# Performance work log

Hardware: AMD Instinct MI355X
Metric: run time of the kernel (lower is better)

Reference implementation:

```python
import jax, jax.numpy as jnp
from jax import lax
import numpy as np

B, N, C, T = 64, 25, 128, 256
EPS = 1e-5


def setup_inputs() -> dict:
    key = jax.random.key(0)
    ks = jax.random.split(key, 4)
    x = jax.random.normal(ks[0], (B, N, C, T), dtype=jnp.float32)
    adj = jax.random.uniform(ks[1], (N, N), dtype=jnp.float32)
    # row-normalize adjacency like a typical GCN propagation matrix
    adj = adj / jnp.sum(adj, axis=1, keepdims=True)
    # xavier-uniform-ish linear weight [out, in]
    lim = float(np.sqrt(6.0 / (C + C)))
    W_gcn = jax.random.uniform(ks[2], (C, C), minval=-lim, maxval=lim, dtype=jnp.float32)
    b_gcn = jnp.zeros((C,), jnp.float32)
    W_conv = jax.random.normal(ks[3], (C, C, 3), dtype=jnp.float32) * (1.0 / np.sqrt(3 * C))
    b_conv = jnp.zeros((C,), jnp.float32)
    return dict(
        x=x, adj=adj, W_gcn=W_gcn, b_gcn=b_gcn, W_conv=W_conv, b_conv=b_conv,
        tc_gamma=jnp.ones((C,), jnp.float32), tc_beta=jnp.zeros((C,), jnp.float32),
        tc_mean=jnp.zeros((C,), jnp.float32), tc_var=jnp.ones((C,), jnp.float32),
        bn_gamma=jnp.ones((C,), jnp.float32), bn_beta=jnp.zeros((C,), jnp.float32),
        bn_mean=jnp.zeros((C,), jnp.float32), bn_var=jnp.ones((C,), jnp.float32),
    )


def _bn(x, gamma, beta, mean, var, axis):
    # eval-mode batchnorm over channel `axis`
    shape = [1] * x.ndim
    shape[axis] = -1
    g = gamma.reshape(shape)
    b = beta.reshape(shape)
    m = mean.reshape(shape)
    v = var.reshape(shape)
    return g * (x - m) * lax.rsqrt(v + EPS) + b


def reference(x, adj, W_gcn, b_gcn, W_conv, b_conv,
              tc_gamma, tc_beta, tc_mean, tc_var,
              bn_gamma, bn_beta, bn_mean, bn_var):
    # x: [B, N, C, T]; in_channels == out_channels so residual is identity
    b_, n_, c_, t_ = x.shape
    residual = x
    # spatial GCN for all timesteps at once: linear over feature dim, then adj matmul over nodes
    h = jnp.einsum('bnct,oc->bnot', x, W_gcn) + b_gcn[None, None, :, None]
    h = jnp.einsum('mn,bnot->bmot', adj, h)  # [B, N, C, T]
    # temporal conv1d over T for every (batch, node) pair at once
    hc = h.reshape(b_ * n_, c_, t_)
    y = lax.conv_general_dilated(hc, W_conv, window_strides=(1,), padding=[(1, 1)],
                                 dimension_numbers=('NCH', 'OIH', 'NCH'))
    y = y + b_conv[None, :, None]
    y = _bn(y, tc_gamma, tc_beta, tc_mean, tc_var, axis=1)
    y = jax.nn.relu(y)
    y = y.reshape(b_, n_, c_, t_)
    # residual add, block batchnorm over channels, relu
    y = y + residual
    y = _bn(y, bn_gamma, bn_beta, bn_mean, bn_var, axis=2)
    y = jax.nn.relu(y)
    return y
```

## Files before the change

### kernel.cpp

```cpp
#include <hip/hip_runtime.h>
#include <hip/hip_bf16.h>
#include <stdint.h>

#define Bn 64
#define Nn 25
#define Cn 128
#define Tn 256
#define EPSC 1e-5f

typedef short bf16x8 __attribute__((ext_vector_type(8)));
typedef float f32x4 __attribute__((ext_vector_type(4)));
typedef int   i32x4 __attribute__((ext_vector_type(4)));

static constexpr size_t X2T_BYTES  = (size_t)Bn * Nn * Tn * Cn * 2;
static constexpr size_t WEFF_OFF   = X2T_BYTES;
static constexpr size_t WEFF_BYTES = (size_t)3 * 128 * 128 * 2;
static constexpr size_t EPI_OFF    = WEFF_OFF + WEFF_BYTES;
static constexpr size_t ROWSUM_OFF = EPI_OFF + (size_t)7 * 128 * 4;
static constexpr size_t ZPAGE_OFF  = ROWSUM_OFF + 256;
static constexpr size_t WS_NEEDED  = ZPAGE_OFF + 256;

__device__ __forceinline__ uint16_t f2bf(float f) {
    uint32_t u = __builtin_bit_cast(uint32_t, f);
    u = (u + 0x7FFFu + ((u >> 16) & 1u)) >> 16;
    return (uint16_t)u;
}

__device__ __forceinline__ void dma16(const void* gsrc, void* ldst) {
    __builtin_amdgcn_global_load_lds(
        (const __attribute__((address_space(1))) unsigned int*)gsrc,
        (__attribute__((address_space(3))) unsigned int*)ldst, 16, 0, 0);
}

__global__ __launch_bounds__(128) void prep_kernel(
    const float* __restrict__ adj, const float* __restrict__ Wg,
    const float* __restrict__ bg,  const float* __restrict__ Wc,
    const float* __restrict__ bc,
    const float* __restrict__ tg,  const float* __restrict__ tb_,
    const float* __restrict__ tm,  const float* __restrict__ tv,
    const float* __restrict__ bng, const float* __restrict__ bnb,
    const float* __restrict__ bnm, const float* __restrict__ bnv,
    uint16_t* __restrict__ weff, float* __restrict__ epi, float* __restrict__ rowsum,
    uint32_t* __restrict__ zpage)
{
    int blk = blockIdx.x;
    int tid = threadIdx.x;
    if (blk < 384) {
        int k = blk >> 7, o = blk & 127;
        float acc = 0.f;
        for (int i = 0; i < 128; ++i) {
            float wc = Wc[(o * 128 + i) * 3 + k];
            acc = fmaf(wc, Wg[i * 128 + tid], acc);
        }
        weff[((size_t)(k * 128 + o)) * 128 + tid] = f2bf(acc);
    } else {
        int o = tid;
        float b0 = 0.f, b1 = 0.f, b2 = 0.f;
        for (int i = 0; i < 128; ++i) {
            float g = bg[i];
            b0 = fmaf(Wc[(o * 128 + i) * 3 + 0], g, b0);
            b1 = fmaf(Wc[(o * 128 + i) * 3 + 1], g, b1);
            b2 = fmaf(Wc[(o * 128 + i) * 3 + 2], g, b2);
        }
        float a1  = tg[o] * rsqrtf(tv[o] + EPSC);
        float c1p = tb_[o] - a1 * tm[o] + a1 * bc[o];
        float a2  = bng[o] * rsqrtf(bnv[o] + EPSC);
        float c2  = bnb[o] - a2 * bnm[o];
        epi[0 * 128 + o] = a1;
        epi[1 * 128 + o] = c1p;
        epi[2 * 128 + o] = a2;
        epi[3 * 128 + o] = c2;
        epi[4 * 128 + o] = a1 * b0;
        epi[5 * 128 + o] = a1 * b1;
        epi[6 * 128 + o] = a1 * b2;
        if (tid < Nn) {
            float s = 0.f;
            for (int n = 0; n < Nn; ++n) s += adj[tid * Nn + n];
            rowsum[tid] = s;
        }
        if (tid < 64) zpage[tid] = 0u;
    }
}

__global__ __launch_bounds__(256) void adjmix_kernel(
    const float* __restrict__ x, const float* __restrict__ adj,
    uint16_t* __restrict__ x2t)
{
    __shared__ float adjs[Nn * Nn];
    __shared__ float tr[2][2][32][33];

    int bid = blockIdx.x;
    int b  = bid >> 5;
    int rem = bid & 31;
    int cb = rem >> 3, tb = rem & 7;
    int c0 = cb * 32, t0 = tb * 32;
    int tid = threadIdx.x;

    for (int i = tid; i < Nn * Nn; i += 256) adjs[i] = adj[i];
    __syncthreads();

    int cl = tid >> 3;
    int t4 = (tid & 7) * 4;

    float acc[Nn][4];
#pragma unroll
    for (int m = 0; m < Nn; ++m)
#pragma unroll
        for (int j = 0; j < 4; ++j) acc[m][j] = 0.f;

    for (int n = 0; n < Nn; ++n) {
        const float4 v = *reinterpret_cast<const float4*>(
            x + (((size_t)(b * Nn + n) * Cn + c0 + cl) * Tn + t0 + t4));
#pragma unroll
        for (int m = 0; m < Nn; ++m) {
            float a = adjs[m * Nn + n];
            acc[m][0] = fmaf(a, v.x, acc[m][0]);
            acc[m][1] = fmaf(a, v.y, acc[m][1]);
            acc[m][2] = fmaf(a, v.z, acc[m][2]);
            acc[m][3] = fmaf(a, v.w, acc[m][3]);
        }
    }

    int h    = tid & 127;
    int half = tid >> 7;
    int trow = h >> 2;
    int cq   = h & 3;

#pragma unroll
    for (int p = 0; p < 13; ++p) {
        int m0  = 2 * p;
        int buf = p & 1;
#pragma unroll
        for (int j = 0; j < 4; ++j) tr[buf][0][cl][t4 + j] = acc[m0][j];
        if (m0 + 1 < Nn) {
#pragma unroll
            for (int j = 0; j < 4; ++j) tr[buf][1][cl][t4 + j] = acc[m0 + 1][j];
        }
        __syncthreads();
        int mm = m0 + half;
        if (mm < Nn) {
            i32x4 u;
#pragma unroll
            for (int k2 = 0; k2 < 4; ++k2) {
                uint32_t lo16 = f2bf(tr[buf][half][cq * 8 + 2 * k2 + 0][trow]);
                uint32_t hi16 = f2bf(tr[buf][half][cq * 8 + 2 * k2 + 1][trow]);
                u[k2] = (int)(lo16 | (hi16 << 16));
            }
            size_t elem = ((size_t)(b * Nn + mm) * Tn + (t0 + trow)) * Cn + c0 + cq * 8;
            *reinterpret_cast<i32x4*>(x2t + elem) = u;
        }
    }
}

__global__ __launch_bounds__(256, 2) void conv_kernel(
    const uint16_t* __restrict__ x2t, const uint16_t* __restrict__ weff,
    const float* __restrict__ x, const float* __restrict__ epi,
    const float* __restrict__ rowsum, const char* __restrict__ zpage,
    float* __restrict__ out)
{
    constexpr int ROWB = 256;
    constexpr int BUFB = 34 * ROWB;
    __shared__ uint16_t lds[2 * 34 * 128];
    char* ldsb = (char*)lds;

    int bid = blockIdx.x;
    int bm  = bid >> 1;
    int th  = bid & 1;
    int m   = bm % Nn;
    int T0  = th * 128;

    int tid = threadIdx.x;
    int w  = tid >> 6;
    int l  = tid & 63;
    int lo = l & 15;
    int hi = l >> 4;
    int o0 = w * 32;

    const char*  xp2 = (const char*)x2t + (size_t)bm * Tn * Cn * 2;
    const short* wp  = (const short*)weff;

    bf16x8 bw[3][4][2];
#pragma unroll
    for (int kk = 0; kk < 3; ++kk)
#pragma unroll
        for (int cc = 0; cc < 4; ++cc)
#pragma unroll
            for (int f = 0; f < 2; ++f) {
                int o = o0 + f * 16 + lo;
                bw[kk][cc][f] = *reinterpret_cast<const bf16x8*>(
                    wp + ((size_t)(kk * 128 + o)) * 128 + cc * 32 + hi * 8);
            }

    float a1[2], c1[2], a2[2], c2v[2], g0[2], g1[2], g2[2];
#pragma unroll
    for (int f = 0; f < 2; ++f) {
        int o = o0 + f * 16 + lo;
        a1[f]  = epi[0 * 128 + o];
        c1[f]  = epi[1 * 128 + o];
        a2[f]  = epi[2 * 128 + o];
        c2v[f] = epi[3 * 128 + o];
        g0[f]  = epi[4 * 128 + o];
        g1[f]  = epi[5 * 128 + o];
        g2[f]  = epi[6 * 128 + o];
    }
    float rs = rowsum[m];
    const size_t obase = (size_t)bm * Cn;

    auto stage = [&](int it, int bufByte) {
        int t0 = T0 + it * 32;
#pragma unroll
        for (int oi = 0; oi < 2; ++oi) {
            int op = w + oi * 4;
            int rowbase = op * 4;
            int r  = rowbase + (l >> 4);
            int cg = l & 15;
            int gt = t0 - 1 + r;
            int sc = cg ^ (r & 7);
            const char* src = (gt >= 0 && gt < Tn)
                ? xp2 + ((size_t)gt * Cn + sc * 8) * 2
                : zpage + sc * 16;
            dma16(src, ldsb + bufByte + rowbase * ROWB);
        }
        if (w == 0 && l < 32) {
            int rowbase = 32;
            int r  = rowbase + (l >> 4);
            int cg = l & 15;
            int gt = t0 - 1 + r;
            int sc = cg ^ (r & 7);
            const char* src = (gt >= 0 && gt < Tn)
                ? xp2 + ((size_t)gt * Cn + sc * 8) * 2
                : zpage + sc * 16;
            dma16(src, ldsb + bufByte + rowbase * ROWB);
        }
    };

    int cur = 0;
    stage(0, 0);
    asm volatile("s_waitcnt vmcnt(0)" ::: "memory");
    __syncthreads();

    for (int it = 0; it < 4; ++it) {
        int nxt = cur ^ 1;
        if (it < 3) stage(it + 1, nxt * BUFB);

        int tq = T0 + it * 32;

        f32x4 r4[2][2];
        size_t idx4[2][2];
#pragma unroll
        for (int j = 0; j < 2; ++j)
#pragma unroll
            for (int f = 0; f < 2; ++f) {
                int o   = o0 + f * 16 + lo;
                int tb4 = tq + j * 16 + hi * 4;
                idx4[j][f] = (obase + o) * Tn + tb4;
                r4[j][f] = *reinterpret_cast<const f32x4*>(x + idx4[j][f]);
            }

        f32x4 acc[2][2];
#pragma unroll
        for (int j = 0; j < 2; ++j)
#pragma unroll
            for (int f = 0; f < 2; ++f) acc[j][f] = (f32x4){0.f, 0.f, 0.f, 0.f};

#pragma unroll
        for (int kk = 0; kk < 3; ++kk)
#pragma unroll
            for (int cc = 0; cc < 4; ++cc) {
                bf16x8 af[2];
#pragma unroll
                for (int j = 0; j < 2; ++j) {
                    int lrow  = j * 16 + lo + kk;
                    int lbyte = cur * BUFB + lrow * ROWB +
                                ((cc * 64 + hi * 16) ^ ((lrow & 7) << 4));
                    af[j] = *reinterpret_cast<const bf16x8*>(ldsb + lbyte);
                }
#pragma unroll
                for (int j = 0; j < 2; ++j)
#pragma unroll
                    for (int f = 0; f < 2; ++f)
                        acc[j][f] = __builtin_amdgcn_mfma_f32_16x16x32_bf16(
                            af[j], bw[kk][cc][f], acc[j][f], 0, 0, 0);
            }

        asm volatile("s_waitcnt vmcnt(0)" ::: "memory");
        __syncthreads();

#pragma unroll
        for (int j = 0; j < 2; ++j)
#pragma unroll
            for (int f = 0; f < 2; ++f) {
                int tb4 = tq + j * 16 + hi * 4;
                f32x4 ov;
#pragma unroll
                for (int qq = 0; qq < 4; ++qq) {
                    int t = tb4 + qq;
                    float gbv = g1[f];
                    if (t > 0)      gbv += g0[f];
                    if (t < Tn - 1) gbv += g2[f];
                    float z = fmaxf(fmaf(a1[f], acc[j][f][qq], fmaf(rs, gbv, c1[f])), 0.f);
                    ov[qq] = fmaxf(fmaf(a2[f], z + r4[j][f][qq], c2v[f]), 0.f);
                }
                *reinterpret_cast<f32x4*>(out + idx4[j][f]) = ov;
            }

        cur = nxt;
    }
}

extern "C" void kernel_launch(void* const* d_in, const int* in_sizes, int n_in,
                              void* d_out, int out_size, void* d_ws, size_t ws_size,
                              hipStream_t stream) {
    const float* x    = (const float*)d_in[0];
    const float* adj  = (const float*)d_in[1];
    const float* Wg   = (const float*)d_in[2];
    const float* bg   = (const float*)d_in[3];
    const float* Wc   = (const float*)d_in[4];
    const float* bc   = (const float*)d_in[5];
    const float* tg   = (const float*)d_in[6];
    const float* tb_  = (const float*)d_in[7];
    const float* tm   = (const float*)d_in[8];
    const float* tv   = (const float*)d_in[9];
    const float* bng  = (const float*)d_in[10];
    const float* bnb  = (const float*)d_in[11];
    const float* bnm  = (const float*)d_in[12];
    const float* bnv  = (const float*)d_in[13];

    if (ws_size < WS_NEEDED) return;

    char* ws = (char*)d_ws;
    uint16_t* x2t    = (uint16_t*)ws;
    uint16_t* weff   = (uint16_t*)(ws + WEFF_OFF);
    float*    epi    = (float*)(ws + EPI_OFF);
    float*    rowsum = (float*)(ws + ROWSUM_OFF);
    char*     zpage  = ws + ZPAGE_OFF;
    float*    out    = (float*)d_out;

    prep_kernel<<<385, 128, 0, stream>>>(adj, Wg, bg, Wc, bc, tg, tb_, tm, tv,
                                         bng, bnb, bnm, bnv, weff, epi, rowsum,
                                         (uint32_t*)zpage);
    adjmix_kernel<<<2048, 256, 0, stream>>>(x, adj, x2t);
    conv_kernel<<<Bn * Nn * 2, 256, 0, stream>>>(x2t, weff, x, epi, rowsum, zpage, out);
}
```

Before: 221.1 us.

## Triple-buffer conv LDS staging and process full time axis per block

Each conv block now covers all 256 timesteps of one (batch, node) pair instead of half, so the grid is halved and the per-block weight and epilogue setup is amortised over eight tiles. LDS staging goes from double to triple buffering with a prefetch distance of two tiles. The per-iteration full vmcnt(0) wait plus syncthreads becomes one raw s_barrier, relying on the in-order vector-memory counter that the compiler's wait on the residual loads already forces. The cost is fewer blocks in flight across the GPU, more LDS per block, and a subtle dependency on implicit wait ordering for correctness.

Measured after the change: 214.0 us. 3.2% less time.

```diff
diff --git a/kernel.cpp b/kernel.cpp
--- a/kernel.cpp
+++ b/kernel.cpp
@@ -160,14 +160,11 @@
 {
     constexpr int ROWB = 256;
     constexpr int BUFB = 34 * ROWB;
-    __shared__ uint16_t lds[2 * 34 * 128];
+    __shared__ uint16_t lds[3 * 34 * 128];
     char* ldsb = (char*)lds;
 
     int bid = blockIdx.x;
-    int bm  = bid >> 1;
-    int th  = bid & 1;
-    int m   = bm % Nn;
-    int T0  = th * 128;
+    int m   = bid % Nn;
 
     int tid = threadIdx.x;
     int w  = tid >> 6;
@@ -176,7 +173,7 @@
     int hi = l >> 4;
     int o0 = w * 32;
 
-    const char*  xp2 = (const char*)x2t + (size_t)bm * Tn * Cn * 2;
+    const char*  xp2 = (const char*)x2t + (size_t)bid * Tn * Cn * 2;
     const short* wp  = (const short*)weff;
 
     bf16x8 bw[3][4][2];
@@ -204,46 +201,46 @@
         g2[f]  = epi[6 * 128 + o];
     }
     float rs = rowsum[m];
-    const size_t obase = (size_t)bm * Cn;
-
-    auto stage = [&](int it, int bufByte) {
-        int t0 = T0 + it * 32;
+    const size_t obase = (size_t)bid * Cn;
+
+    auto stage = [&](int q, int slot) {
+        int tbase = q * 32 - 1;
+        char* dstbase = ldsb + slot * BUFB;
 #pragma unroll
         for (int oi = 0; oi < 2; ++oi) {
-            int op = w + oi * 4;
-            int rowbase = op * 4;
+            int rowbase = (w + oi * 4) * 4;
             int r  = rowbase + (l >> 4);
             int cg = l & 15;
-            int gt = t0 - 1 + r;
+            int gt = tbase + r;
             int sc = cg ^ (r & 7);
             const char* src = (gt >= 0 && gt < Tn)
                 ? xp2 + ((size_t)gt * Cn + sc * 8) * 2
                 : zpage + sc * 16;
-            dma16(src, ldsb + bufByte + rowbase * ROWB);
+            dma16(src, dstbase + rowbase * ROWB);
         }
         if (w == 0 && l < 32) {
             int rowbase = 32;
             int r  = rowbase + (l >> 4);
             int cg = l & 15;
-            int gt = t0 - 1 + r;
+            int gt = tbase + r;
             int sc = cg ^ (r & 7);
             const char* src = (gt >= 0 && gt < Tn)
                 ? xp2 + ((size_t)gt * Cn + sc * 8) * 2
                 : zpage + sc * 16;
-            dma16(src, ldsb + bufByte + rowbase * ROWB);
+            dma16(src, dstbase + rowbase * ROWB);
         }
     };
 
-    int cur = 0;
+    asm volatile("" ::: "memory");
     stage(0, 0);
-    asm volatile("s_waitcnt vmcnt(0)" ::: "memory");
-    __syncthreads();
-
-    for (int it = 0; it < 4; ++it) {
-        int nxt = cur ^ 1;
-        if (it < 3) stage(it + 1, nxt * BUFB);
-
-        int tq = T0 + it * 32;
+    stage(1, 1);
+    asm volatile("s_waitcnt vmcnt(2)" ::: "memory");
+    __builtin_amdgcn_s_barrier();
+    asm volatile("" ::: "memory");
+
+    int slot = 0;
+    for (int it = 0; it < 8; ++it) {
+        int tq = it * 32;
 
         f32x4 r4[2][2];
         size_t idx4[2][2];
@@ -256,6 +253,14 @@
                 idx4[j][f] = (obase + o) * Tn + tb4;
                 r4[j][f] = *reinterpret_cast<const f32x4*>(x + idx4[j][f]);
             }
+        __builtin_amdgcn_sched_barrier(0);
+
+        {
+            int q  = it + 2; if (q > 7) q = 7;
+            int s2 = slot >= 1 ? slot - 1 : 2;
+            stage(q, s2);
+        }
+        __builtin_amdgcn_sched_barrier(0);
 
         f32x4 acc[2][2];
 #pragma unroll
@@ -271,7 +276,7 @@
 #pragma unroll
                 for (int j = 0; j < 2; ++j) {
                     int lrow  = j * 16 + lo + kk;
-                    int lbyte = cur * BUFB + lrow * ROWB +
+                    int lbyte = slot * BUFB + lrow * ROWB +
                                 ((cc * 64 + hi * 16) ^ ((lrow & 7) << 4));
                     af[j] = *reinterpret_cast<const bf16x8*>(ldsb + lbyte);
                 }
@@ -282,9 +287,6 @@
                         acc[j][f] = __builtin_amdgcn_mfma_f32_16x16x32_bf16(
                             af[j], bw[kk][cc][f], acc[j][f], 0, 0, 0);
             }
-
-        asm volatile("s_waitcnt vmcnt(0)" ::: "memory");
-        __syncthreads();
 
 #pragma unroll
         for (int j = 0; j < 2; ++j)
@@ -304,8 +306,14 @@
                 *reinterpret_cast<f32x4*>(out + idx4[j][f]) = ov;
             }
 
-        cur = nxt;
-    }
+        asm volatile("" ::: "memory");
+        __builtin_amdgcn_s_barrier();
+        asm volatile("" ::: "memory");
+
+        slot = slot + 1 == 3 ? 0 : slot + 1;
+    }
+
+    asm volatile("s_waitcnt vmcnt(0)" ::: "memory");
 }
 
 extern "C" void kernel_launch(void* const* d_in, const int* in_sizes, int n_in,
@@ -340,5 +348,5 @@
                                          bng, bnb, bnm, bnv, weff, epi, rowsum,
                                          (uint32_t*)zpage);
     adjmix_kernel<<<2048, 256, 0, stream>>>(x, adj, x2t);
-    conv_kernel<<<Bn * Nn * 2, 256, 0, stream>>>(x2t, weff, x, epi, rowsum, zpage, out);
-}
+    conv_kernel<<<Bn * Nn, 256, 0, stream>>>(x2t, weff, x, epi, rowsum, zpage, out);
+}
```

## Load whole conv tile up front and make adjmix transpose warp-local

Applied to the files above, without the earlier changes.

The conv kernel now issues DMA loads for the full 130-row bf16 input tile (all 128 timesteps plus halo) before loading weights. It then runs the four time sub-blocks with no per-iteration wait or barrier, replacing the double-buffered staging loop. The adjmix kernel's transpose goes through per-wavefront shared buffers written as float4, so the block-wide __syncthreads between write and read is removed. The intent is to cut barrier and pipeline stalls, at the cost of more LDS per conv block (about 33KB), which may lower occupancy. The warp-local transpose also relies on wavefront lockstep without an explicit barrier.

Result: slower. 237.2 us (+7.3%).

```diff
diff --git a/kernel.cpp b/kernel.cpp
--- a/kernel.cpp
+++ b/kernel.cpp
@@ -87,7 +87,7 @@
     uint16_t* __restrict__ x2t)
 {
     __shared__ float adjs[Nn * Nn];
-    __shared__ float tr[2][2][32][33];
+    __shared__ float trw[4][2][2][8][36];
 
     int bid = blockIdx.x;
     int b  = bid >> 5;
@@ -121,32 +121,31 @@
         }
     }
 
-    int h    = tid & 127;
-    int half = tid >> 7;
-    int trow = h >> 2;
-    int cq   = h & 3;
+    int w  = tid >> 6;
+    int l  = tid & 63;
+    int lc = cl & 7;
+    int h  = l >> 5;
+    int tt = l & 31;
 
 #pragma unroll
     for (int p = 0; p < 13; ++p) {
         int m0  = 2 * p;
         int buf = p & 1;
-#pragma unroll
-        for (int j = 0; j < 4; ++j) tr[buf][0][cl][t4 + j] = acc[m0][j];
-        if (m0 + 1 < Nn) {
-#pragma unroll
-            for (int j = 0; j < 4; ++j) tr[buf][1][cl][t4 + j] = acc[m0 + 1][j];
-        }
-        __syncthreads();
-        int mm = m0 + half;
+        *reinterpret_cast<f32x4*>(&trw[w][buf][0][lc][t4]) =
+            (f32x4){acc[m0][0], acc[m0][1], acc[m0][2], acc[m0][3]};
+        if (m0 + 1 < Nn)
+            *reinterpret_cast<f32x4*>(&trw[w][buf][1][lc][t4]) =
+                (f32x4){acc[m0 + 1][0], acc[m0 + 1][1], acc[m0 + 1][2], acc[m0 + 1][3]};
+        int mm = m0 + h;
         if (mm < Nn) {
             i32x4 u;
 #pragma unroll
             for (int k2 = 0; k2 < 4; ++k2) {
-                uint32_t lo16 = f2bf(tr[buf][half][cq * 8 + 2 * k2 + 0][trow]);
-                uint32_t hi16 = f2bf(tr[buf][half][cq * 8 + 2 * k2 + 1][trow]);
+                uint32_t lo16 = f2bf(trw[w][buf][h][2 * k2 + 0][tt]);
+                uint32_t hi16 = f2bf(trw[w][buf][h][2 * k2 + 1][tt]);
                 u[k2] = (int)(lo16 | (hi16 << 16));
             }
-            size_t elem = ((size_t)(b * Nn + mm) * Tn + (t0 + trow)) * Cn + c0 + cq * 8;
+            size_t elem = ((size_t)(b * Nn + mm) * Tn + (t0 + tt)) * Cn + c0 + 8 * w;
             *reinterpret_cast<i32x4*>(x2t + elem) = u;
         }
     }
@@ -159,8 +158,7 @@
     float* __restrict__ out)
 {
     constexpr int ROWB = 256;
-    constexpr int BUFB = 34 * ROWB;
-    __shared__ uint16_t lds[2 * 34 * 128];
+    __shared__ uint16_t lds[130 * 128];
     char* ldsb = (char*)lds;
 
     int bid = blockIdx.x;
@@ -178,6 +176,20 @@
 
     const char*  xp2 = (const char*)x2t + (size_t)bm * Tn * Cn * 2;
     const short* wp  = (const short*)weff;
+
+#pragma unroll
+    for (int p = 0; p < 9; ++p) {
+        int chunk = p * 256 + tid;
+        if (chunk < 2080) {
+            int lrow = chunk >> 4, cg = chunk & 15;
+            int gt = T0 - 1 + lrow;
+            int sc = cg ^ (lrow & 7);
+            const char* src = (gt >= 0 && gt < Tn)
+                ? xp2 + ((size_t)gt * Cn + sc * 8) * 2
+                : zpage + sc * 16;
+            dma16(src, ldsb + lrow * ROWB + cg * 16);
+        }
+    }
 
     bf16x8 bw[3][4][2];
 #pragma unroll
@@ -206,44 +218,12 @@
     float rs = rowsum[m];
     const size_t obase = (size_t)bm * Cn;
 
-    auto stage = [&](int it, int bufByte) {
-        int t0 = T0 + it * 32;
-#pragma unroll
-        for (int oi = 0; oi < 2; ++oi) {
-            int op = w + oi * 4;
-            int rowbase = op * 4;
-            int r  = rowbase + (l >> 4);
-            int cg = l & 15;
-            int gt = t0 - 1 + r;
-            int sc = cg ^ (r & 7);
-            const char* src = (gt >= 0 && gt < Tn)
-                ? xp2 + ((size_t)gt * Cn + sc * 8) * 2
-                : zpage + sc * 16;
-            dma16(src, ldsb + bufByte + rowbase * ROWB);
-        }
-        if (w == 0 && l < 32) {
-            int rowbase = 32;
-            int r  = rowbase + (l >> 4);
-            int cg = l & 15;
-            int gt = t0 - 1 + r;
-            int sc = cg ^ (r & 7);
-            const char* src = (gt >= 0 && gt < Tn)
-                ? xp2 + ((size_t)gt * Cn + sc * 8) * 2
-                : zpage + sc * 16;
-            dma16(src, ldsb + bufByte + rowbase * ROWB);
-        }
-    };
-
-    int cur = 0;
-    stage(0, 0);
     asm volatile("s_waitcnt vmcnt(0)" ::: "memory");
     __syncthreads();
 
-    for (int it = 0; it < 4; ++it) {
-        int nxt = cur ^ 1;
-        if (it < 3) stage(it + 1, nxt * BUFB);
-
-        int tq = T0 + it * 32;
+#pragma unroll
+    for (int tq4 = 0; tq4 < 4; ++tq4) {
+        int tq = T0 + tq4 * 32;
 
         f32x4 r4[2][2];
         size_t idx4[2][2];
@@ -270,8 +250,8 @@
                 bf16x8 af[2];
 #pragma unroll
                 for (int j = 0; j < 2; ++j) {
-                    int lrow  = j * 16 + lo + kk;
-                    int lbyte = cur * BUFB + lrow * ROWB +
+                    int lrow  = tq4 * 32 + j * 16 + lo + kk;
+                    int lbyte = lrow * ROWB +
                                 ((cc * 64 + hi * 16) ^ ((lrow & 7) << 4));
                     af[j] = *reinterpret_cast<const bf16x8*>(ldsb + lbyte);
                 }
@@ -282,9 +262,6 @@
                         acc[j][f] = __builtin_amdgcn_mfma_f32_16x16x32_bf16(
                             af[j], bw[kk][cc][f], acc[j][f], 0, 0, 0);
             }
-
-        asm volatile("s_waitcnt vmcnt(0)" ::: "memory");
-        __syncthreads();
 
 #pragma unroll
         for (int j = 0; j < 2; ++j)
@@ -303,8 +280,6 @@
                 }
                 *reinterpret_cast<f32x4*>(out + idx4[j][f]) = ov;
             }
-
-        cur = nxt;
     }
 }
 
```

## Stage residual tiles through LDS via async DMA and use one block per (b,n)

Applied to the files above, without the earlier changes.

The conv kernel now prefetches the fp32 residual tile for each 32-step time chunk into LDS with the same async DMA double-buffer used for the bf16 activations. This replaces direct global loads that stalled the epilogue. The grid is halved so each block walks all 256 timesteps in 8 iterations, which saves a second reload of the weight fragments and halo rows. The cost is much more LDS per block (about 50KB for the double buffer), which may lower occupancy, and fewer blocks in flight.

Result: faster. 204.1 us (-7.7%).

```diff
diff --git a/kernel.cpp b/kernel.cpp
--- a/kernel.cpp
+++ b/kernel.cpp
@@ -159,15 +159,13 @@
     float* __restrict__ out)
 {
     constexpr int ROWB = 256;
-    constexpr int BUFB = 34 * ROWB;
-    __shared__ uint16_t lds[2 * 34 * 128];
-    char* ldsb = (char*)lds;
+    constexpr int X2TB = 34 * ROWB;
+    constexpr int RESB = 128 * 128;
+    constexpr int BUFB = X2TB + RESB;
+    __shared__ __align__(16) char ldsb[2 * BUFB];
 
     int bid = blockIdx.x;
-    int bm  = bid >> 1;
-    int th  = bid & 1;
-    int m   = bm % Nn;
-    int T0  = th * 128;
+    int m   = bid % Nn;
 
     int tid = threadIdx.x;
     int w  = tid >> 6;
@@ -176,8 +174,9 @@
     int hi = l >> 4;
     int o0 = w * 32;
 
-    const char*  xp2 = (const char*)x2t + (size_t)bm * Tn * Cn * 2;
-    const short* wp  = (const short*)weff;
+    const char* xp2 = (const char*)x2t + (size_t)bid * Tn * Cn * 2;
+    const char* xre = (const char*)x   + (size_t)bid * Cn * Tn * 4;
+    const short* wp = (const short*)weff;
 
     bf16x8 bw[3][4][2];
 #pragma unroll
@@ -204,14 +203,13 @@
         g2[f]  = epi[6 * 128 + o];
     }
     float rs = rowsum[m];
-    const size_t obase = (size_t)bm * Cn;
+    const size_t obase = (size_t)bid * Cn;
 
     auto stage = [&](int it, int bufByte) {
-        int t0 = T0 + it * 32;
+        int t0 = it * 32;
 #pragma unroll
         for (int oi = 0; oi < 2; ++oi) {
-            int op = w + oi * 4;
-            int rowbase = op * 4;
+            int rowbase = (w + oi * 4) * 4;
             int r  = rowbase + (l >> 4);
             int cg = l & 15;
             int gt = t0 - 1 + r;
@@ -232,6 +230,15 @@
                 : zpage + sc * 16;
             dma16(src, ldsb + bufByte + rowbase * ROWB);
         }
+#pragma unroll
+        for (int oi = 0; oi < 4; ++oi) {
+            int p    = w * 4 + oi;
+            int orow = p * 8 + (l >> 3);
+            int cg   = l & 7;
+            int sc   = cg ^ (orow & 7);
+            const char* src = xre + (size_t)orow * (Tn * 4) + (size_t)t0 * 4 + sc * 16;
+            dma16(src, ldsb + bufByte + X2TB + p * 1024);
+        }
     };
 
     int cur = 0;
@@ -239,23 +246,11 @@
     asm volatile("s_waitcnt vmcnt(0)" ::: "memory");
     __syncthreads();
 
-    for (int it = 0; it < 4; ++it) {
+    for (int it = 0; it < 8; ++it) {
         int nxt = cur ^ 1;
-        if (it < 3) stage(it + 1, nxt * BUFB);
-
-        int tq = T0 + it * 32;
-
-        f32x4 r4[2][2];
-        size_t idx4[2][2];
-#pragma unroll
-        for (int j = 0; j < 2; ++j)
-#pragma unroll
-            for (int f = 0; f < 2; ++f) {
-                int o   = o0 + f * 16 + lo;
-                int tb4 = tq + j * 16 + hi * 4;
-                idx4[j][f] = (obase + o) * Tn + tb4;
-                r4[j][f] = *reinterpret_cast<const f32x4*>(x + idx4[j][f]);
-            }
+        if (it < 7) stage(it + 1, nxt * BUFB);
+
+        int tq = it * 32;
 
         f32x4 acc[2][2];
 #pragma unroll
@@ -283,14 +278,15 @@
                             af[j], bw[kk][cc][f], acc[j][f], 0, 0, 0);
             }
 
-        asm volatile("s_waitcnt vmcnt(0)" ::: "memory");
-        __syncthreads();
-
 #pragma unroll
         for (int j = 0; j < 2; ++j)
 #pragma unroll
             for (int f = 0; f < 2; ++f) {
-                int tb4 = tq + j * 16 + hi * 4;
+                int o    = o0 + f * 16 + lo;
+                int tb4  = tq + j * 16 + hi * 4;
+                int rbyte = cur * BUFB + X2TB + o * 128 +
+                            ((j * 64 + hi * 16) ^ ((o & 7) << 4));
+                f32x4 r4 = *reinterpret_cast<const f32x4*>(ldsb + rbyte);
                 f32x4 ov;
 #pragma unroll
                 for (int qq = 0; qq < 4; ++qq) {
@@ -299,11 +295,13 @@
                     if (t > 0)      gbv += g0[f];
                     if (t < Tn - 1) gbv += g2[f];
                     float z = fmaxf(fmaf(a1[f], acc[j][f][qq], fmaf(rs, gbv, c1[f])), 0.f);
-                    ov[qq] = fmaxf(fmaf(a2[f], z + r4[j][f][qq], c2v[f]), 0.f);
+                    ov[qq] = fmaxf(fmaf(a2[f], z + r4[qq], c2v[f]), 0.f);
                 }
-                *reinterpret_cast<f32x4*>(out + idx4[j][f]) = ov;
+                *reinterpret_cast<f32x4*>(out + (obase + o) * Tn + tb4) = ov;
             }
 
+        asm volatile("s_waitcnt vmcnt(0)" ::: "memory");
+        __syncthreads();
         cur = nxt;
     }
 }
@@ -340,5 +338,5 @@
                                          bng, bnb, bnm, bnv, weff, epi, rowsum,
                                          (uint32_t*)zpage);
     adjmix_kernel<<<2048, 256, 0, stream>>>(x, adj, x2t);
-    conv_kernel<<<Bn * Nn * 2, 256, 0, stream>>>(x2t, weff, x, epi, rowsum, zpage, out);
-}
+    conv_kernel<<<Bn * Nn, 256, 0, stream>>>(x2t, weff, x, epi, rowsum, zpage, out);
+}
```
